# Kernel tuning notes

Hardware: AMD Instinct MI355X
Metric: run time of the kernel (lower is better)

Reference implementation:

```python
import jax, jax.numpy as jnp
import numpy as np

B, S, D = 8, 4096, 1024       # batch, seq_len, d_model
WIN = 257                     # window_size (odd): keys [i-128, i+128]
HALF = WIN // 2               # 128
BL = 256                      # block length for banded attention (BL >= HALF, S % BL == 0)


def setup_inputs() -> dict:
    key = jax.random.key(0)
    ks = jax.random.split(key, 7)
    s = 0.02
    return {
        "x":  jax.random.normal(ks[0], (B, S, D), jnp.float32),
        "Wq": jax.random.normal(ks[1], (D, D), jnp.float32) * s,
        "bq": jnp.zeros((D,), jnp.float32),
        "Wk": jax.random.normal(ks[2], (D, D), jnp.float32) * s,
        "bk": jnp.zeros((D,), jnp.float32),
        "Wv": jax.random.normal(ks[3], (D, D), jnp.float32) * s,
        "bv": jnp.zeros((D,), jnp.float32),
    }


def _blockify(t, nb):
    # t: [B, S, D] -> [B, nb, 3*BL, D]; for block b, keys from blocks b-1, b, b+1 (zero-padded at edges)
    b, s, d = t.shape
    tp = jnp.pad(t, ((0, 0), (BL, BL), (0, 0)))
    tb = tp.reshape(b, nb + 2, BL, d)
    return jnp.concatenate([tb[:, :-2], tb[:, 1:-1], tb[:, 2:]], axis=2)


def _local_attention(q, k, v):
    # Faithful vectorized form of the per-token sliding-window loop:
    # for each i: keys/values from [max(0, i-HALF), min(S, i+HALF+1)), scaled-dot softmax.
    b, s, d = q.shape
    nb = s // BL
    qb = q.reshape(b, nb, BL, d)
    kb = _blockify(k, nb)                          # [B, nb, 3BL, D]
    vb = _blockify(v, nb)
    scale = 1.0 / np.sqrt(d).astype(np.float32)    # d_model ** 0.5 (scaled_dot)
    scores = jnp.einsum('bnqd,bnkd->bnqk', qb, kb) * scale  # [B, nb, BL, 3BL]

    blk = jnp.arange(nb)[:, None, None]
    r = jnp.arange(BL)[None, :, None]
    c = jnp.arange(3 * BL)[None, None, :]
    i = blk * BL + r                               # global query position
    j = (blk - 1) * BL + c                         # global key position
    rel = j - i
    valid = (rel >= -HALF) & (rel <= HALF) & (j >= 0) & (j < s)  # [nb, BL, 3BL]

    scores = jnp.where(valid[None], scores, -jnp.inf)
    weights = jax.nn.softmax(scores, axis=-1)
    out = jnp.einsum('bnqk,bnkd->bnqd', weights, vb)
    return out.reshape(b, s, d)


def reference(x, Wq, bq, Wk, bk, Wv, bv) -> jnp.ndarray:
    q = x @ Wq + bq
    k = x @ Wk + bk
    v = x @ Wv + bv
    return _local_attention(q, k, v)
```

## Files before the change

### kernel.cpp

```cpp
#include <hip/hip_runtime.h>
#include <hip/hip_fp16.h>
#include <cstdint>


#define DEV __device__ __forceinline__

typedef _Float16 f16x8 __attribute__((ext_vector_type(8)));
typedef _Float16 f16x4 __attribute__((ext_vector_type(4)));
typedef float    f32x4 __attribute__((ext_vector_type(4)));

DEV _Float16 f2h(float f) { return (_Float16)f; }

DEV void gl16(const void* g, void* l) {
  __builtin_amdgcn_global_load_lds(
      (const __attribute__((address_space(1))) void*)(uintptr_t)g,
      (__attribute__((address_space(3))) void*)(uintptr_t)l, 16, 0, 0);
}

#define MFMA16(a, b, c) __builtin_amdgcn_mfma_f32_16x16x32_f16((a), (b), (c), 0, 0, 0)

__global__ __launch_bounds__(256) void k_cvt_x(const float* __restrict__ x,
                                               _Float16* __restrict__ xh) {
  size_t i = ((size_t)blockIdx.x * 256 + threadIdx.x) * 8;
  float4 f0 = *(const float4*)(x + i);
  float4 f1 = *(const float4*)(x + i + 4);
  f16x8 o;
  o[0] = f2h(f0.x); o[1] = f2h(f0.y); o[2] = f2h(f0.z); o[3] = f2h(f0.w);
  o[4] = f2h(f1.x); o[5] = f2h(f1.y); o[6] = f2h(f1.z); o[7] = f2h(f1.w);
  *(f16x8*)(xh + i) = o;
}

__global__ __launch_bounds__(256) void k_cvt_w(const float* __restrict__ Wq,
                                               const float* __restrict__ Wk,
                                               const float* __restrict__ Wv,
                                               _Float16* __restrict__ wt) {
  __shared__ float tile[64][65];
  const int z = blockIdx.z;
  const int n0 = blockIdx.x * 64, k0 = blockIdx.y * 64;
  const float* W = (z == 0) ? Wq : (z == 1) ? Wk : Wv;
  const int tid = threadIdx.x;
  const int r0 = tid >> 4;
  const int c4 = (tid & 15) * 4;
#pragma unroll
  for (int rr = 0; rr < 4; ++rr) {
    int r = r0 + rr * 16;
    float4 v = *(const float4*)(W + (size_t)(k0 + r) * 1024 + n0 + c4);
    tile[r][c4 + 0] = v.x; tile[r][c4 + 1] = v.y;
    tile[r][c4 + 2] = v.z; tile[r][c4 + 3] = v.w;
  }
  __syncthreads();
  _Float16* out = wt + (size_t)z * 1048576;
#pragma unroll
  for (int rr = 0; rr < 4; ++rr) {
    int n = r0 + rr * 16;
    f16x4 o;
#pragma unroll
    for (int jj = 0; jj < 4; ++jj) o[jj] = f2h(tile[c4 + jj][n]);
    *(f16x4*)(out + (size_t)(n0 + n) * 1024 + k0 + c4) = o;
  }
}

__global__ __launch_bounds__(512, 2) void k_gemm_qkv(
    const _Float16* __restrict__ xh, const _Float16* __restrict__ wt,
    const float* __restrict__ bq, const float* __restrict__ bk,
    const float* __restrict__ bv, _Float16* __restrict__ qh,
    _Float16* __restrict__ kh, _Float16* __restrict__ v8) {
  __shared__ _Float16 L[65536];

  const int bid = blockIdx.x;
  const int wg = (bid & 7) * 192 + (bid >> 3);
  const int mt = wg / 12, nt = wg % 12;
  const int gm0 = mt * 256;
  const int gn0 = nt * 256;

  const int tid = threadIdx.x;
  const int w = tid >> 6, l = tid & 63;
  const int ln = l & 15, quad = l >> 4;
  const int wm = w >> 2, wn = w & 3;
  const int lr = l >> 3;
  const int kc = ((l & 7) ^ lr) * 8;
  const int swz = ln & 7;

  auto stageA = [&](int it, int h) {
    const _Float16* src =
        xh + (size_t)(gm0 + h * 128 + w * 8 + lr) * 1024 + it * 64 + kc;
    _Float16* dst = L + (it & 1) * 32768 + (h * 128 + w * 8) * 64;
    gl16(src, dst);
    gl16(src + 64 * 1024, dst + 64 * 64);
  };
  auto stageB = [&](int it, int h) {
    const _Float16* src =
        wt + (size_t)(gn0 + h * 128 + w * 8 + lr) * 1024 + it * 64 + kc;
    _Float16* dst = L + (it & 1) * 32768 + 16384 + (h * 128 + w * 8) * 64;
    gl16(src, dst);
    gl16(src + 64 * 1024, dst + 64 * 64);
  };

#define RD(base, r, ko) \
  (*(const f16x8*)((base) + (size_t)(r) * 64 + (((ko) ^ swz) * 8)))

  f32x4 acc[8][4] = {};
  f16x8 aA[2][4], bb0[2][2], bb1[2][2];

  stageA(0, 0); stageA(0, 1); stageB(0, 0); stageB(0, 1);
  stageB(1, 0); stageB(1, 1);
  asm volatile("s_waitcnt vmcnt(4)" ::: "memory");
  __builtin_amdgcn_s_barrier();

#pragma unroll 2
  for (int t = 0; t < 16; ++t) {
    const _Float16* Ab = L + (t & 1) * 32768;
    const _Float16* Bb = Ab + 16384;
    const int rA = wm * 128 + ln;
    const int rB = wn * 64 + ln;

#pragma unroll
    for (int i = 0; i < 4; ++i) {
      aA[0][i] = RD(Ab, rA + i * 16, quad);
      aA[1][i] = RD(Ab, rA + i * 16, quad + 4);
    }
#pragma unroll
    for (int j = 0; j < 2; ++j) {
      bb0[0][j] = RD(Bb, rB + j * 16, quad);
      bb0[1][j] = RD(Bb, rB + j * 16, quad + 4);
    }
    if (t + 1 < 16) stageA(t + 1, 0);
    __builtin_amdgcn_s_barrier();
    asm volatile("s_waitcnt lgkmcnt(0)" ::: "memory");
    __builtin_amdgcn_sched_barrier(0);
    __builtin_amdgcn_s_setprio(1);
#pragma unroll
    for (int s = 0; s < 2; ++s)
#pragma unroll
      for (int i = 0; i < 4; ++i)
#pragma unroll
        for (int j = 0; j < 2; ++j)
          acc[i][j] = MFMA16(aA[s][i], bb0[s][j], acc[i][j]);
    __builtin_amdgcn_s_setprio(0);
    __builtin_amdgcn_s_barrier();

#pragma unroll
    for (int j = 0; j < 2; ++j) {
      bb1[0][j] = RD(Bb, rB + 32 + j * 16, quad);
      bb1[1][j] = RD(Bb, rB + 32 + j * 16, quad + 4);
    }
    if (t + 1 < 16) stageA(t + 1, 1);
    __builtin_amdgcn_s_barrier();
    asm volatile("s_waitcnt lgkmcnt(0)" ::: "memory");
    __builtin_amdgcn_sched_barrier(0);
    __builtin_amdgcn_s_setprio(1);
#pragma unroll
    for (int s = 0; s < 2; ++s)
#pragma unroll
      for (int i = 0; i < 4; ++i)
#pragma unroll
        for (int j = 0; j < 2; ++j)
          acc[i][2 + j] = MFMA16(aA[s][i], bb1[s][j], acc[i][2 + j]);
    __builtin_amdgcn_s_setprio(0);
    __builtin_amdgcn_s_barrier();

#pragma unroll
    for (int i = 0; i < 4; ++i) {
      aA[0][i] = RD(Ab, rA + 64 + i * 16, quad);
      aA[1][i] = RD(Ab, rA + 64 + i * 16, quad + 4);
    }
    if (t + 2 < 16) stageB(t + 2, 0);
    __builtin_amdgcn_s_barrier();
    asm volatile("s_waitcnt lgkmcnt(0)" ::: "memory");
    __builtin_amdgcn_sched_barrier(0);
    __builtin_amdgcn_s_setprio(1);
#pragma unroll
    for (int s = 0; s < 2; ++s)
#pragma unroll
      for (int i = 0; i < 4; ++i)
#pragma unroll
        for (int j = 0; j < 2; ++j)
          acc[4 + i][2 + j] = MFMA16(aA[s][i], bb1[s][j], acc[4 + i][2 + j]);
    __builtin_amdgcn_s_setprio(0);
    __builtin_amdgcn_s_barrier();

    if (t + 2 < 16) stageB(t + 2, 1);
    __builtin_amdgcn_s_setprio(1);
#pragma unroll
    for (int s = 0; s < 2; ++s)
#pragma unroll
      for (int i = 0; i < 4; ++i)
#pragma unroll
        for (int j = 0; j < 2; ++j)
          acc[4 + i][j] = MFMA16(aA[s][i], bb0[s][j], acc[4 + i][j]);
    __builtin_amdgcn_s_setprio(0);
    if (t + 2 < 16)
      asm volatile("s_waitcnt vmcnt(4)" ::: "memory");
    else
      asm volatile("s_waitcnt vmcnt(0)" ::: "memory");
    __builtin_amdgcn_s_barrier();
  }
#undef RD

  const int z2 = gn0 >> 10;
  const int colz = (gn0 & 1023) + wn * 64;
  const int row0 = gm0 + wm * 128;
  if (z2 != 2) {
    const float* bias = z2 ? bk : bq;
    _Float16* outp = z2 ? kh : qh;
#pragma unroll
    for (int j = 0; j < 4; ++j) {
      float bb = bias[colz + j * 16 + ln];
#pragma unroll
      for (int i = 0; i < 8; ++i) {
        int row = row0 + i * 16 + quad * 4;
        size_t base = (size_t)row * 1024 + colz + j * 16 + ln;
#pragma unroll
        for (int r = 0; r < 4; ++r)
          outp[base + (size_t)r * 1024] = f2h(acc[i][j][r] + bb);
      }
    }
  } else {
#pragma unroll
    for (int j = 0; j < 4; ++j) {
      float bb = bv[colz + j * 16 + ln];
#pragma unroll
      for (int i = 0; i < 8; ++i) {
        int rr = row0 + i * 16 + quad * 4;
        int col = colz + j * 16 + ln;
        f16x4 o;
#pragma unroll
        for (int r = 0; r < 4; ++r) o[r] = f2h(acc[i][j][r] + bb);
        *(f16x4*)(v8 + (size_t)(rr >> 3) * 8192 + (size_t)col * 8 + (rr & 7)) = o;
      }
    }
  }
}

__global__ __launch_bounds__(512) void k_scores(const _Float16* __restrict__ qh,
                                                const _Float16* __restrict__ kh,
                                                _Float16* __restrict__ ph) {
  __shared__ _Float16 lQ[2][128 * 64];
  __shared__ _Float16 lK[2][384 * 64];
  __shared__ float redM[4][128];
  __shared__ float redS[4][128];
  const int t = blockIdx.x, b = blockIdx.y;
  const int i0 = t * 128, k0 = i0 - 128;
  const int tid = threadIdx.x, w = tid >> 6, l = tid & 63;
  const int ln = l & 15, quad = l >> 4;
  const int wm2 = w >> 2, wn4 = w & 3;
  const _Float16* qrow = qh + (size_t)b * 4096 * 1024;
  const _Float16* krow = kh + (size_t)b * 4096 * 1024;
  const int kc = ((l & 7) ^ (l >> 3)) * 8;
  const int swz = ln & 7;

  auto stage = [&](int it) {
    int buf = it & 1;
#pragma unroll
    for (int c = 0; c < 2; ++c) {
      int cid = w * 2 + c;
      int rl = cid * 8 + (l >> 3);
      gl16(qrow + (size_t)(i0 + rl) * 1024 + it * 64 + kc, &lQ[buf][cid * 512]);
    }
#pragma unroll
    for (int c = 0; c < 6; ++c) {
      int cid = w * 6 + c;
      int rl = cid * 8 + (l >> 3);
      int gr = min(max(k0 + rl, 0), 4095);
      gl16(krow + (size_t)gr * 1024 + it * 64 + kc, &lK[buf][cid * 512]);
    }
  };

  f32x4 s[4][6] = {};

  stage(0);
  asm volatile("s_waitcnt vmcnt(0)" ::: "memory");
  __builtin_amdgcn_s_barrier();

  for (int it = 0; it < 16; ++it) {
    int buf = it & 1;
    if (it + 1 < 16) stage(it + 1);
    f16x8 af[2][4], bf[2][6];
#pragma unroll
    for (int i = 0; i < 4; ++i) {
      int r = wm2 * 64 + i * 16 + ln;
      af[0][i] = *(const f16x8*)(&lQ[buf][r * 64 + ((quad ^ swz) * 8)]);
      af[1][i] = *(const f16x8*)(&lQ[buf][r * 64 + (((quad + 4) ^ swz) * 8)]);
    }
#pragma unroll
    for (int j = 0; j < 6; ++j) {
      int r = wn4 * 96 + j * 16 + ln;
      bf[0][j] = *(const f16x8*)(&lK[buf][r * 64 + ((quad ^ swz) * 8)]);
      bf[1][j] = *(const f16x8*)(&lK[buf][r * 64 + (((quad + 4) ^ swz) * 8)]);
    }
    asm volatile("s_waitcnt lgkmcnt(0)" ::: "memory");
    __builtin_amdgcn_sched_barrier(0);
    __builtin_amdgcn_s_setprio(1);
#pragma unroll
    for (int ss = 0; ss < 2; ++ss)
#pragma unroll
      for (int i = 0; i < 4; ++i)
#pragma unroll
        for (int j = 0; j < 6; ++j)
          s[i][j] = MFMA16(af[ss][i], bf[ss][j], s[i][j]);
    __builtin_amdgcn_s_setprio(0);
    asm volatile("s_waitcnt vmcnt(0)" ::: "memory");
    __builtin_amdgcn_s_barrier();
  }

  const float scale = 0.03125f;
  float mrow[4][4];
#pragma unroll
  for (int i = 0; i < 4; ++i)
#pragma unroll
    for (int r = 0; r < 4; ++r) mrow[i][r] = -1e30f;
#pragma unroll
  for (int j = 0; j < 6; ++j) {
    int jc = k0 + wn4 * 96 + j * 16 + ln;
    bool cval = (jc >= 0) && (jc < 4096);
#pragma unroll
    for (int i = 0; i < 4; ++i)
#pragma unroll
      for (int r = 0; r < 4; ++r) {
        int iq = i0 + wm2 * 64 + i * 16 + quad * 4 + r;
        int rel = jc - iq;
        bool val = cval && (rel >= -128) && (rel <= 128);
        float sc = val ? s[i][j][r] * scale : -1e30f;
        s[i][j][r] = sc;
        mrow[i][r] = fmaxf(mrow[i][r], sc);
      }
  }
#pragma unroll
  for (int i = 0; i < 4; ++i)
#pragma unroll
    for (int r = 0; r < 4; ++r)
#pragma unroll
      for (int m = 1; m < 16; m <<= 1)
        mrow[i][r] = fmaxf(mrow[i][r], __shfl_xor(mrow[i][r], m));
  if (ln == 0) {
#pragma unroll
    for (int i = 0; i < 4; ++i)
#pragma unroll
      for (int r = 0; r < 4; ++r)
        redM[wn4][wm2 * 64 + i * 16 + quad * 4 + r] = mrow[i][r];
  }
  __syncthreads();
  float mf[4][4];
#pragma unroll
  for (int i = 0; i < 4; ++i)
#pragma unroll
    for (int r = 0; r < 4; ++r) {
      int row = wm2 * 64 + i * 16 + quad * 4 + r;
      mf[i][r] = fmaxf(fmaxf(redM[0][row], redM[1][row]),
                       fmaxf(redM[2][row], redM[3][row]));
    }
  float srow[4][4] = {};
#pragma unroll
  for (int j = 0; j < 6; ++j)
#pragma unroll
    for (int i = 0; i < 4; ++i)
#pragma unroll
      for (int r = 0; r < 4; ++r) {
        float e = __builtin_exp2f((s[i][j][r] - mf[i][r]) * 1.44269504f);
        s[i][j][r] = e;
        srow[i][r] += e;
      }
#pragma unroll
  for (int i = 0; i < 4; ++i)
#pragma unroll
    for (int r = 0; r < 4; ++r)
#pragma unroll
      for (int m = 1; m < 16; m <<= 1) srow[i][r] += __shfl_xor(srow[i][r], m);
  if (ln == 0) {
#pragma unroll
    for (int i = 0; i < 4; ++i)
#pragma unroll
      for (int r = 0; r < 4; ++r)
        redS[wn4][wm2 * 64 + i * 16 + quad * 4 + r] = srow[i][r];
  }
  __syncthreads();
  float inv[4][4];
#pragma unroll
  for (int i = 0; i < 4; ++i)
#pragma unroll
    for (int r = 0; r < 4; ++r) {
      int row = wm2 * 64 + i * 16 + quad * 4 + r;
      inv[i][r] = 1.0f / (redS[0][row] + redS[1][row] + redS[2][row] + redS[3][row]);
    }
  _Float16* pt = ph + (size_t)(b * 32 + t) * 128 * 384;
#pragma unroll
  for (int j = 0; j < 6; ++j) {
    int col = wn4 * 96 + j * 16 + ln;
    int oct = col >> 3, e = col & 7;
#pragma unroll
    for (int i = 0; i < 4; ++i)
#pragma unroll
      for (int r = 0; r < 4; ++r) {
        int row = wm2 * 64 + i * 16 + quad * 4 + r;
        pt[row * 384 + ((oct ^ (row & 7)) << 3) + e] = f2h(s[i][j][r] * inv[i][r]);
      }
  }
}

__global__ __launch_bounds__(512) void k_pv(const _Float16* __restrict__ ph,
                                            const _Float16* __restrict__ v8,
                                            float* __restrict__ out) {
  __shared__ _Float16 lP[128 * 384];
  __shared__ _Float16 lV[2][48 * 32 * 8];
  const int t = blockIdx.x, b = blockIdx.y;
  const int tid = threadIdx.x, w = tid >> 6, l = tid & 63;
  const int ln = l & 15, quad = l >> 4;
  const int wq = w >> 1, wn2 = w & 1;
  const _Float16* pt = ph + (size_t)(b * 32 + t) * 128 * 384;
  const _Float16* vb = v8 + (size_t)b * 4194304;
  const int g0 = (t * 128 - 128) >> 3;

  auto stageV = [&](int c) {
    int buf = c & 1;
    int n0 = c * 32;
#pragma unroll
    for (int cc = 0; cc < 3; ++cc) {
      int ob = w * 6 + cc * 2;
      int oct = ob + (l >> 5);
      int g = min(max(g0 + oct, 0), 511);
      gl16(vb + (size_t)g * 8192 + (size_t)(n0 + (l & 31)) * 8,
           &lV[buf][ob * 256]);
    }
  };

  #pragma unroll
  for (int c = 0; c < 12; ++c)
    gl16(pt + ((size_t)(c * 512 + w * 64 + l)) * 8, &lP[(c * 512 + w * 64) * 8]);
  stageV(0);
  stageV(1);
  asm volatile("s_waitcnt vmcnt(3)" ::: "memory");
  __builtin_amdgcn_s_barrier();

  for (int c = 0; c < 32; ++c) {
    int buf = c & 1;
    if (c + 1 < 32) stageV(c + 1);
    f32x4 acc[2] = {};
#pragma unroll
    for (int ks = 0; ks < 12; ++ks) {
      int o = ks * 4 + quad;
      int rA0 = wq * 32 + ln;
      int rA1 = rA0 + 16;
      f16x8 a0 = *(const f16x8*)(&lP[rA0 * 384 + ((o ^ (rA0 & 7)) << 3)]);
      f16x8 a1 = *(const f16x8*)(&lP[rA1 * 384 + ((o ^ (rA1 & 7)) << 3)]);
      f16x8 bv = *(const f16x8*)(&lV[buf][(o * 32 + wn2 * 16 + ln) * 8]);
      acc[0] = MFMA16(a0, bv, acc[0]);
      acc[1] = MFMA16(a1, bv, acc[1]);
    }
    int col = c * 32 + wn2 * 16 + ln;
#pragma unroll
    for (int i = 0; i < 2; ++i) {
      int row = t * 128 + wq * 32 + i * 16 + quad * 4;
      size_t base = ((size_t)b * 4096 + row) * 1024 + col;
#pragma unroll
      for (int r = 0; r < 4; ++r) out[base + (size_t)r * 1024] = acc[i][r];
    }
    if (c + 1 < 32) {
      asm volatile("s_waitcnt vmcnt(8)" ::: "memory");
      __builtin_amdgcn_s_barrier();
    }
  }
}

extern "C" void kernel_launch(void* const* d_in, const int* in_sizes, int n_in,
                              void* d_out, int out_size, void* d_ws, size_t ws_size,
                              hipStream_t stream) {
  const float* x  = (const float*)d_in[0];
  const float* Wq = (const float*)d_in[1];
  const float* bq = (const float*)d_in[2];
  const float* Wk = (const float*)d_in[3];
  const float* bk = (const float*)d_in[4];
  const float* Wv = (const float*)d_in[5];
  const float* bv = (const float*)d_in[6];
  float* out = (float*)d_out;

  _Float16* ws = (_Float16*)d_ws;
  _Float16* xh = ws;
  _Float16* wt = ws + 33554432;
  _Float16* qh = ws + 36700160;
  _Float16* kh = ws + 70254592;
  _Float16* v8 = ws + 103809024;
  _Float16* ph = ws;

  k_cvt_x<<<16384, 256, 0, stream>>>(x, xh);
  k_cvt_w<<<dim3(16, 16, 3), 256, 0, stream>>>(Wq, Wk, Wv, wt);
  k_gemm_qkv<<<dim3(1536), 512, 0, stream>>>(xh, wt, bq, bk, bv, qh, kh, v8);
  k_scores<<<dim3(32, 8), 512, 0, stream>>>(qh, kh, ph);
  k_pv<<<dim3(32, 8), 512, 0, stream>>>(ph, v8, out);
}
```

Baseline: 556.4 us.

## Fuse score-softmax and PV kernels so probabilities stay in LDS

Merges the scores/softmax kernel and the P·V kernel into a single attention kernel. The normalized probability tile is written to shared memory and consumed there directly, instead of being stored to a global workspace and reloaded. The shared memory is one aliased buffer that is reused in turn for Q/K staging, the reduction scratch, P and double-buffered V. This removes a roughly 25 MB global round trip and one kernel launch. In exchange it uses about 147 KB of LDS per block and depends on careful barrier and vmcnt ordering between the overlapping regions.

Measured after the change: 524.0 us. 1.06x faster.

```diff
diff --git a/kernel.cpp b/kernel.cpp
--- a/kernel.cpp
+++ b/kernel.cpp
@@ -232,13 +232,11 @@
   }
 }
 
-__global__ __launch_bounds__(512) void k_scores(const _Float16* __restrict__ qh,
-                                                const _Float16* __restrict__ kh,
-                                                _Float16* __restrict__ ph) {
-  __shared__ _Float16 lQ[2][128 * 64];
-  __shared__ _Float16 lK[2][384 * 64];
-  __shared__ float redM[4][128];
-  __shared__ float redS[4][128];
+__global__ __launch_bounds__(512, 2) void k_attn(const _Float16* __restrict__ qh,
+                                                 const _Float16* __restrict__ kh,
+                                                 const _Float16* __restrict__ v8,
+                                                 float* __restrict__ out) {
+  __shared__ _Float16 smem[73728];
   const int t = blockIdx.x, b = blockIdx.y;
   const int i0 = t * 128, k0 = i0 - 128;
   const int tid = threadIdx.x, w = tid >> 6, l = tid & 63;
@@ -246,6 +244,7 @@
   const int wm2 = w >> 2, wn4 = w & 3;
   const _Float16* qrow = qh + (size_t)b * 4096 * 1024;
   const _Float16* krow = kh + (size_t)b * 4096 * 1024;
+  const _Float16* vb = v8 + (size_t)b * 4194304;
   const int kc = ((l & 7) ^ (l >> 3)) * 8;
   const int swz = ln & 7;
 
@@ -255,14 +254,16 @@
     for (int c = 0; c < 2; ++c) {
       int cid = w * 2 + c;
       int rl = cid * 8 + (l >> 3);
-      gl16(qrow + (size_t)(i0 + rl) * 1024 + it * 64 + kc, &lQ[buf][cid * 512]);
+      gl16(qrow + (size_t)(i0 + rl) * 1024 + it * 64 + kc,
+           &smem[buf * 8192 + cid * 512]);
     }
 #pragma unroll
     for (int c = 0; c < 6; ++c) {
       int cid = w * 6 + c;
       int rl = cid * 8 + (l >> 3);
       int gr = min(max(k0 + rl, 0), 4095);
-      gl16(krow + (size_t)gr * 1024 + it * 64 + kc, &lK[buf][cid * 512]);
+      gl16(krow + (size_t)gr * 1024 + it * 64 + kc,
+           &smem[16384 + buf * 24576 + cid * 512]);
     }
   };
 
@@ -279,14 +280,14 @@
 #pragma unroll
     for (int i = 0; i < 4; ++i) {
       int r = wm2 * 64 + i * 16 + ln;
-      af[0][i] = *(const f16x8*)(&lQ[buf][r * 64 + ((quad ^ swz) * 8)]);
-      af[1][i] = *(const f16x8*)(&lQ[buf][r * 64 + (((quad + 4) ^ swz) * 8)]);
+      af[0][i] = *(const f16x8*)(&smem[buf * 8192 + r * 64 + ((quad ^ swz) * 8)]);
+      af[1][i] = *(const f16x8*)(&smem[buf * 8192 + r * 64 + (((quad + 4) ^ swz) * 8)]);
     }
 #pragma unroll
     for (int j = 0; j < 6; ++j) {
       int r = wn4 * 96 + j * 16 + ln;
-      bf[0][j] = *(const f16x8*)(&lK[buf][r * 64 + ((quad ^ swz) * 8)]);
-      bf[1][j] = *(const f16x8*)(&lK[buf][r * 64 + (((quad + 4) ^ swz) * 8)]);
+      bf[0][j] = *(const f16x8*)(&smem[16384 + buf * 24576 + r * 64 + ((quad ^ swz) * 8)]);
+      bf[1][j] = *(const f16x8*)(&smem[16384 + buf * 24576 + r * 64 + (((quad + 4) ^ swz) * 8)]);
     }
     asm volatile("s_waitcnt lgkmcnt(0)" ::: "memory");
     __builtin_amdgcn_sched_barrier(0);
@@ -303,6 +304,8 @@
     __builtin_amdgcn_s_barrier();
   }
 
+  float* redM = (float*)(&smem[65536]);
+  float* redS = redM + 512;
   const float scale = 0.03125f;
   float mrow[4][4];
 #pragma unroll
@@ -337,7 +340,7 @@
     for (int i = 0; i < 4; ++i)
 #pragma unroll
       for (int r = 0; r < 4; ++r)
-        redM[wn4][wm2 * 64 + i * 16 + quad * 4 + r] = mrow[i][r];
+        redM[wn4 * 128 + wm2 * 64 + i * 16 + quad * 4 + r] = mrow[i][r];
   }
   __syncthreads();
   float mf[4][4];
@@ -346,8 +349,8 @@
 #pragma unroll
     for (int r = 0; r < 4; ++r) {
       int row = wm2 * 64 + i * 16 + quad * 4 + r;
-      mf[i][r] = fmaxf(fmaxf(redM[0][row], redM[1][row]),
-                       fmaxf(redM[2][row], redM[3][row]));
+      mf[i][r] = fmaxf(fmaxf(redM[row], redM[128 + row]),
+                       fmaxf(redM[256 + row], redM[384 + row]));
     }
   float srow[4][4] = {};
 #pragma unroll
@@ -371,7 +374,7 @@
     for (int i = 0; i < 4; ++i)
 #pragma unroll
       for (int r = 0; r < 4; ++r)
-        redS[wn4][wm2 * 64 + i * 16 + quad * 4 + r] = srow[i][r];
+        redS[wn4 * 128 + wm2 * 64 + i * 16 + quad * 4 + r] = srow[i][r];
   }
   __syncthreads();
   float inv[4][4];
@@ -380,9 +383,8 @@
 #pragma unroll
     for (int r = 0; r < 4; ++r) {
       int row = wm2 * 64 + i * 16 + quad * 4 + r;
-      inv[i][r] = 1.0f / (redS[0][row] + redS[1][row] + redS[2][row] + redS[3][row]);
-    }
-  _Float16* pt = ph + (size_t)(b * 32 + t) * 128 * 384;
+      inv[i][r] = 1.0f / (redS[row] + redS[128 + row] + redS[256 + row] + redS[384 + row]);
+    }
 #pragma unroll
   for (int j = 0; j < 6; ++j) {
     int col = wn4 * 96 + j * 16 + ln;
@@ -392,23 +394,14 @@
 #pragma unroll
       for (int r = 0; r < 4; ++r) {
         int row = wm2 * 64 + i * 16 + quad * 4 + r;
-        pt[row * 384 + ((oct ^ (row & 7)) << 3) + e] = f2h(s[i][j][r] * inv[i][r]);
+        smem[row * 384 + ((oct ^ (row & 7)) << 3) + e] = f2h(s[i][j][r] * inv[i][r]);
       }
   }
-}
-
-__global__ __launch_bounds__(512) void k_pv(const _Float16* __restrict__ ph,
-                                            const _Float16* __restrict__ v8,
-                                            float* __restrict__ out) {
-  __shared__ _Float16 lP[128 * 384];
-  __shared__ _Float16 lV[2][48 * 32 * 8];
-  const int t = blockIdx.x, b = blockIdx.y;
-  const int tid = threadIdx.x, w = tid >> 6, l = tid & 63;
-  const int ln = l & 15, quad = l >> 4;
+  __syncthreads();
+
   const int wq = w >> 1, wn2 = w & 1;
-  const _Float16* pt = ph + (size_t)(b * 32 + t) * 128 * 384;
-  const _Float16* vb = v8 + (size_t)b * 4194304;
   const int g0 = (t * 128 - 128) >> 3;
+  _Float16* lV = &smem[49152];
 
   auto stageV = [&](int c) {
     int buf = c & 1;
@@ -419,13 +412,10 @@
       int oct = ob + (l >> 5);
       int g = min(max(g0 + oct, 0), 511);
       gl16(vb + (size_t)g * 8192 + (size_t)(n0 + (l & 31)) * 8,
-           &lV[buf][ob * 256]);
+           &lV[buf * 12288 + ob * 256]);
     }
   };
 
-  #pragma unroll
-  for (int c = 0; c < 12; ++c)
-    gl16(pt + ((size_t)(c * 512 + w * 64 + l)) * 8, &lP[(c * 512 + w * 64) * 8]);
   stageV(0);
   stageV(1);
   asm volatile("s_waitcnt vmcnt(3)" ::: "memory");
@@ -433,16 +423,16 @@
 
   for (int c = 0; c < 32; ++c) {
     int buf = c & 1;
-    if (c + 1 < 32) stageV(c + 1);
+    if (c >= 1 && c + 1 < 32) stageV(c + 1);
     f32x4 acc[2] = {};
 #pragma unroll
     for (int ks = 0; ks < 12; ++ks) {
       int o = ks * 4 + quad;
       int rA0 = wq * 32 + ln;
       int rA1 = rA0 + 16;
-      f16x8 a0 = *(const f16x8*)(&lP[rA0 * 384 + ((o ^ (rA0 & 7)) << 3)]);
-      f16x8 a1 = *(const f16x8*)(&lP[rA1 * 384 + ((o ^ (rA1 & 7)) << 3)]);
-      f16x8 bv = *(const f16x8*)(&lV[buf][(o * 32 + wn2 * 16 + ln) * 8]);
+      f16x8 a0 = *(const f16x8*)(&smem[rA0 * 384 + ((o ^ (rA0 & 7)) << 3)]);
+      f16x8 a1 = *(const f16x8*)(&smem[rA1 * 384 + ((o ^ (rA1 & 7)) << 3)]);
+      f16x8 bv = *(const f16x8*)(&lV[buf * 12288 + (o * 32 + wn2 * 16 + ln) * 8]);
       acc[0] = MFMA16(a0, bv, acc[0]);
       acc[1] = MFMA16(a1, bv, acc[1]);
     }
@@ -479,11 +469,9 @@
   _Float16* qh = ws + 36700160;
   _Float16* kh = ws + 70254592;
   _Float16* v8 = ws + 103809024;
-  _Float16* ph = ws;
 
   k_cvt_x<<<16384, 256, 0, stream>>>(x, xh);
   k_cvt_w<<<dim3(16, 16, 3), 256, 0, stream>>>(Wq, Wk, Wv, wt);
   k_gemm_qkv<<<dim3(1536), 512, 0, stream>>>(xh, wt, bq, bk, bv, qh, kh, v8);
-  k_scores<<<dim3(32, 8), 512, 0, stream>>>(qh, kh, ph);
-  k_pv<<<dim3(32, 8), 512, 0, stream>>>(ph, v8, out);
-}
+  k_attn<<<dim3(32, 8), 512, 0, stream>>>(qh, kh, v8, out);
+}
```
